# Performance work log

Measured on AMD Instinct MI355X. Metric: run time of the kernel, lower is better.

Reference implementation:

```python
import math
import jax, jax.numpy as jnp
import numpy as np

MARGIN_SCALER = 0.2
IGNORING_RATE = 0.1
NBITS = 64
TEMPERATURE = 0.1
B, L, E, D = 4096, 32, 512, 64


def setup_inputs() -> dict:
    key = jax.random.key(0)
    k1, k2, k3, k4, k5, k6 = jax.random.split(key, 6)
    return {
        "outputs_h1": jax.random.uniform(k1, (B, D), dtype=jnp.float32),
        "outputs_h2": jax.random.uniform(k2, (B, D), dtype=jnp.float32),
        "caps_embed": jax.random.normal(k3, (B, L, E), dtype=jnp.float32),
        "sim_mat": jax.random.normal(k4, (B, L, 1), dtype=jnp.float32),
        "s_v": jax.random.normal(k5, (B, D), dtype=jnp.float32),
        "s_v2": jax.random.normal(k6, (B, D), dtype=jnp.float32),
        "epochs": 5,
    }


def _cosine_sim(h, eps=1e-5):
    n = jnp.linalg.norm(h, axis=1, keepdims=True)
    a = h / jnp.maximum(n, eps)
    return a @ a.T  # [B, B]


def _self_contrastive_loss(img, tgt, caps_embed, epochs, sim_mat2d):
    batch_size = caps_embed.shape[0]
    w = jax.nn.softmax(sim_mat2d, axis=-1)              # [B, L]
    caps_mean = jnp.einsum('bl,ble->be', w, caps_embed)  # [B, E]
    cos = jnp.clip(_cosine_sim(caps_mean), 1e-6, 1.0 - 1e-6)  # [B, B]
    scores = img @ tgt.T                                 # [B, B]
    d1 = jnp.diag(scores)[:, None]
    cost_s = jnp.maximum((1.0 - cos) * MARGIN_SCALER + scores - d1, 1e-8)
    eye = jnp.eye(batch_size, dtype=cost_s.dtype)
    cost_s = cost_s * (1.0 - eye)  # masked_fill diagonal with 0
    clean_rate = epochs * IGNORING_RATE if epochs * IGNORING_RATE < 1 else 0.99
    k = math.ceil(batch_size * batch_size * (1 - clean_rate))
    thr = jnp.sort(cost_s.reshape(-1))[k - 1]  # k-th smallest (topk largest=False)
    cost_s = jnp.where(cost_s < thr, cost_s, jnp.zeros_like(cost_s))
    return cost_s.sum()


def _quantization_loss(img, nbits, lamda=1.0):
    loss = -lamda * jnp.sum((1.0 / nbits) * jnp.square(img - 0.5), axis=1)
    return loss.mean()


def _distillation_loss(stu, tcher, temperature=TEMPERATURE):
    p_t = jax.nn.log_softmax(tcher / temperature, axis=-1)
    p_s = jax.nn.log_softmax(stu / temperature, axis=-1)
    # KLDivLoss(reduction='sum', log_target=True): sum(exp(target)*(target-input))
    return jnp.sum(jnp.exp(p_t) * (p_t - p_s))


def reference(outputs_h1, outputs_h2, caps_embed, sim_mat, s_v, s_v2, epochs):
    sim2d = jax.lax.stop_gradient(sim_mat[..., 0])  # detach + squeeze(-1)
    loss1 = _self_contrastive_loss(outputs_h1, outputs_h2, caps_embed, epochs, sim2d)
    loss2 = _quantization_loss(outputs_h1, NBITS)
    loss3 = _distillation_loss(s_v2, s_v)
    # AutomaticWeightedLoss(3) with freshly-initialized params = ones(3):
    # sum_i 0.5/p_i^2 * loss_i + log(1 + p_i^2) with p_i = 1
    ln2 = jnp.log(jnp.asarray(2.0, dtype=jnp.float32))
    loss_sum = 0.5 * loss1 + ln2 + 0.5 * loss2 + ln2 + 0.5 * loss3 + ln2
    return loss_sum
```

## Files before the change

kernel.cpp:

```cpp
#include <hip/hip_runtime.h>
#include <hip/hip_bf16.h>

#define TPB 256
#define CTPB 512

using f32x4  = __attribute__((ext_vector_type(4))) float;
using bf16x8 = __attribute__((ext_vector_type(8))) short;

static constexpr int BB = 4096;

static constexpr size_t OFF_AHI  = 0;
static constexpr size_t OFF_D1   = 8388608;
static constexpr size_t OFF_H1   = OFF_D1 + 16384;
static constexpr size_t OFF_GS1  = OFF_H1 + 8192;
static constexpr size_t OFF_L2P  = OFF_GS1 + 16384;
static constexpr size_t OFF_L3P  = OFF_L2P + 8192;
static constexpr size_t OFF_HS   = OFF_L3P + 8192;
static constexpr size_t HS_ONE   = (size_t)BB * 64 * 2;
static constexpr size_t ZERO_OFF = OFF_H1;
static constexpr size_t ZERO_LEN = OFF_L2P - OFF_H1;

__device__ __forceinline__ void bsplit(float x, unsigned short& h, unsigned short& l)
{
    unsigned b = __float_as_uint(x);
    unsigned r = (b + 0x7FFFu + ((b >> 16) & 1u)) >> 16;
    h = (unsigned short)r;
    float hf = __uint_as_float(r << 16);
    float lof = x - hf;
    unsigned b2 = __float_as_uint(lof);
    unsigned r2 = (b2 + 0x7FFFu + ((b2 >> 16) & 1u)) >> 16;
    l = (unsigned short)r2;
}

__device__ __forceinline__ unsigned short b2h(float x)
{
    unsigned b = __float_as_uint(x);
    return (unsigned short)((b + 0x7FFFu + ((b >> 16) & 1u)) >> 16);
}

__device__ __forceinline__ void gload16(const void* g, void* l)
{
    __builtin_amdgcn_global_load_lds((const __attribute__((address_space(1))) void*)g,
                                     (__attribute__((address_space(3))) void*)l,
                                     16, 0, 0);
}

__global__ __launch_bounds__(TPB) void front_k(
    const float* __restrict__ caps, const float* __restrict__ sim,
    unsigned short* __restrict__ ahi,
    const float* __restrict__ h1f, const float* __restrict__ h2f,
    unsigned short* __restrict__ h1hi, unsigned short* __restrict__ h1lo,
    unsigned short* __restrict__ h2hi, unsigned short* __restrict__ h2lo,
    float* __restrict__ d1, const float* __restrict__ sv,
    const float* __restrict__ sv2, double* __restrict__ l2part,
    double* __restrict__ l3part, char* __restrict__ base)
{
    const int blk = (int)blockIdx.x;
    const int tid = threadIdx.x;
    __shared__ float sm[32];
    __shared__ float w[32];
    __shared__ float red[4];
    __shared__ float nrm;
    __shared__ double r2[4], r3[4];

    if (blk < 4096) {
        const int b = blk;
        if (tid < 32) sm[tid] = sim[b * 32 + tid];
        __syncthreads();
        if (tid < 32) {
            float m = -1e30f;
            for (int l = 0; l < 32; ++l) m = fmaxf(m, sm[l]);
            float ssum = 0.f;
            for (int l = 0; l < 32; ++l) ssum += expf(sm[l] - m);
            w[tid] = expf(sm[tid] - m) / ssum;
        }
        __syncthreads();
        const float2* cb2 = (const float2*)(caps + (size_t)b * 32 * 512);
        float cx = 0.f, cy = 0.f;
        for (int l = 0; l < 32; ++l) {
            float wl = w[l];
            float2 v = cb2[l * 256 + tid];
            cx = fmaf(wl, v.x, cx);
            cy = fmaf(wl, v.y, cy);
        }
        float ss = cx * cx + cy * cy;
        #pragma unroll
        for (int off = 32; off; off >>= 1) ss += __shfl_down(ss, off, 64);
        if ((tid & 63) == 0) red[tid >> 6] = ss;
        __syncthreads();
        if (tid == 0) nrm = sqrtf(red[0] + red[1] + red[2] + red[3]);
        __syncthreads();
        float an = fmaxf(nrm, 1e-5f);
        ahi[(size_t)b * 512 + 2 * tid]     = b2h(cx / an);
        ahi[(size_t)b * 512 + 2 * tid + 1] = b2h(cy / an);
    } else if (blk < 5120) {
        const int pb   = blk - 4096;
        const int row  = (pb << 2) + (tid >> 6);
        const int lane = tid & 63;
        const int i    = (row << 6) + lane;
        float x1 = h1f[i], x2 = h2f[i];
        unsigned short h, l;
        bsplit(x1, h, l); h1hi[i] = h; h1lo[i] = l;
        bsplit(x2, h, l); h2hi[i] = h; h2lo[i] = l;
        float p = x1 * x2;
        #pragma unroll
        for (int m = 32; m; m >>= 1) p += __shfl_xor(p, m, 64);
        if (lane == 0) d1[row] = p;
        float xq = x1 - 0.5f;
        double s2 = (double)(xq * xq);
        #pragma unroll
        for (int m = 32; m; m >>= 1) s2 += __shfl_xor(s2, m, 64);
        float xt = sv[i] / 0.1f;
        float xs = sv2[i] / 0.1f;
        float mt = xt, ms = xs;
        #pragma unroll
        for (int m = 32; m; m >>= 1) {
            mt = fmaxf(mt, __shfl_xor(mt, m, 64));
            ms = fmaxf(ms, __shfl_xor(ms, m, 64));
        }
        float et = expf(xt - mt), es = expf(xs - ms);
        float sst = et, sss = es;
        #pragma unroll
        for (int m = 32; m; m >>= 1) { sst += __shfl_xor(sst, m, 64); sss += __shfl_xor(sss, m, 64); }
        float pt = (xt - mt) - logf(sst);
        float ps = (xs - ms) - logf(sss);
        double d3 = (double)((et / sst) * (pt - ps));
        #pragma unroll
        for (int m = 32; m; m >>= 1) d3 += __shfl_xor(d3, m, 64);
        if (lane == 0) { r2[tid >> 6] = s2; r3[tid >> 6] = d3; }
        __syncthreads();
        if (tid == 0) {
            l2part[pb] = r2[0] + r2[1] + r2[2] + r2[3];
            l3part[pb] = r3[0] + r3[1] + r3[2] + r3[3];
        }
    } else {
        unsigned* z = (unsigned*)(base + ZERO_OFF);
        const int n = (int)(ZERO_LEN / 4);
        for (int i2 = (blk - 5120) * TPB + tid; i2 < n; i2 += 8 * TPB) z[i2] = 0u;
    }
}

__global__ __launch_bounds__(CTPB, 1) void cost_pass(
    const unsigned short* __restrict__ ahi,
    const unsigned short* __restrict__ h1hi, const unsigned short* __restrict__ h1lo,
    const unsigned short* __restrict__ h2hi, const unsigned short* __restrict__ h2lo,
    const float* __restrict__ d1,
    unsigned* __restrict__ hist, double* __restrict__ gsum)
{
    __shared__ char lds_raw[131072];
    __shared__ float sD1[128];
    const int tid  = threadIdx.x;
    const int lane = tid & 63;
    const int wid  = tid >> 6;
    const int wr   = wid >> 2;
    const int wc   = wid & 3;

    const int orig = (int)blockIdx.x;
    const int xcd  = orig & 7;
    const int idx  = orig >> 3;
    const int bi   = (((xcd >> 1) << 3) + (idx & 7)) << 7;
    const int bj   = (((xcd & 1) << 4) + (idx >> 3)) << 7;

    f32x4 accC[4][2], accS[4][2];
    #pragma unroll
    for (int m = 0; m < 4; ++m)
        #pragma unroll
        for (int n = 0; n < 2; ++n)
            #pragma unroll
            for (int q = 0; q < 4; ++q) { accC[m][n][q] = 0.f; accS[m][n][q] = 0.f; }

    auto STAGE = [&](int t) {
        char* d = lds_raw + ((size_t)(t & 3) << 15);
        if (t < 8) {
            const int k0b = t << 7;
            #pragma unroll
            for (int q = 0; q < 2; ++q) {
                int o    = (q << 13) + (tid << 4);
                int row  = o >> 7;
                int slot = (o >> 4) & 7;
                int sc   = (slot ^ (row & 7)) << 4;
                gload16((const char*)ahi + (size_t)(bi + row) * 1024 + k0b + sc, d + o);
                gload16((const char*)ahi + (size_t)(bj + row) * 1024 + k0b + sc, d + 16384 + o);
            }
        } else {
            const int k0b = (t - 8) << 6;
            int o    = tid << 4;
            int row  = o >> 6;
            int slot = (o >> 4) & 3;
            int sc   = (slot ^ ((row >> 1) & 3)) << 4;
            size_t ra = (size_t)(bi + row) * 128 + k0b + sc;
            size_t rb = (size_t)(bj + row) * 128 + k0b + sc;
            gload16((const char*)h1hi + ra, d + o);
            gload16((const char*)h1lo + ra, d + 8192 + o);
            gload16((const char*)h2hi + rb, d + 16384 + o);
            gload16((const char*)h2lo + rb, d + 24576 + o);
        }
    };

    STAGE(0);
    STAGE(1);
    #pragma unroll 1
    for (int t = 0; t < 10; ++t) {
        if (t < 8) STAGE(t + 2);
        __builtin_amdgcn_sched_barrier(0);
        if (t < 8)       asm volatile("s_waitcnt vmcnt(8)" ::: "memory");
        else if (t == 8) asm volatile("s_waitcnt vmcnt(4)" ::: "memory");
        else             asm volatile("s_waitcnt vmcnt(0)" ::: "memory");
        __builtin_amdgcn_s_barrier();
        const char* bufb = lds_raw + ((size_t)(t & 3) << 15);
        if (t < 8) {
            #pragma unroll
            for (int ks = 0; ks < 2; ++ks) {
                bf16x8 a_[4], b_[2];
                const int pbase = (ks << 2) + (lane >> 4);
                #pragma unroll
                for (int m = 0; m < 4; ++m) {
                    int row = wr * 64 + m * 16 + (lane & 15);
                    a_[m] = *(const bf16x8*)(bufb + row * 128 + ((pbase ^ (lane & 7)) << 4));
                }
                #pragma unroll
                for (int n = 0; n < 2; ++n) {
                    int row = wc * 32 + n * 16 + (lane & 15);
                    b_[n] = *(const bf16x8*)(bufb + 16384 + row * 128 + ((pbase ^ (lane & 7)) << 4));
                }
                __builtin_amdgcn_s_setprio(1);
                #pragma unroll
                for (int m = 0; m < 4; ++m)
                    #pragma unroll
                    for (int n = 0; n < 2; ++n)
                        accC[m][n] = __builtin_amdgcn_mfma_f32_16x16x32_bf16(a_[m], b_[n], accC[m][n], 0, 0, 0);
                __builtin_amdgcn_s_setprio(0);
            }
        } else {
            const int rdsw = (((lane >> 4) ^ ((lane >> 1) & 3)) << 4);
            bf16x8 ah[4], bh[2], bl[2];
            #pragma unroll
            for (int m = 0; m < 4; ++m)
                ah[m] = *(const bf16x8*)(bufb + (size_t)(wr * 64 + m * 16 + (lane & 15)) * 64 + rdsw);
            #pragma unroll
            for (int n = 0; n < 2; ++n) {
                bh[n] = *(const bf16x8*)(bufb + 16384 + (size_t)(wc * 32 + n * 16 + (lane & 15)) * 64 + rdsw);
                bl[n] = *(const bf16x8*)(bufb + 24576 + (size_t)(wc * 32 + n * 16 + (lane & 15)) * 64 + rdsw);
            }
            __builtin_amdgcn_s_setprio(1);
            #pragma unroll
            for (int m = 0; m < 4; ++m)
                #pragma unroll
                for (int n = 0; n < 2; ++n) {
                    accS[m][n] = __builtin_amdgcn_mfma_f32_16x16x32_bf16(ah[m], bh[n], accS[m][n], 0, 0, 0);
                    accS[m][n] = __builtin_amdgcn_mfma_f32_16x16x32_bf16(ah[m], bl[n], accS[m][n], 0, 0, 0);
                }
            __builtin_amdgcn_s_setprio(0);
            bf16x8 al[4];
            #pragma unroll
            for (int m = 0; m < 4; ++m)
                al[m] = *(const bf16x8*)(bufb + 8192 + (size_t)(wr * 64 + m * 16 + (lane & 15)) * 64 + rdsw);
            __builtin_amdgcn_s_setprio(1);
            #pragma unroll
            for (int m = 0; m < 4; ++m)
                #pragma unroll
                for (int n = 0; n < 2; ++n)
                    accS[m][n] = __builtin_amdgcn_mfma_f32_16x16x32_bf16(al[m], bh[n], accS[m][n], 0, 0, 0);
            __builtin_amdgcn_s_setprio(0);
        }
        __builtin_amdgcn_sched_barrier(0);
    }

    __syncthreads();
    unsigned* lh = (unsigned*)lds_raw;
    float*    ls = (float*)(lds_raw + 32768);
    if (tid < 128) sD1[tid] = d1[bi + tid];
    for (int q = tid; q < 8192; q += CTPB) lh[q] = 0u;
    for (int q = tid; q < 4096; q += CTPB) ls[q] = 0.f;
    __syncthreads();
    unsigned* lhW = lh + (wid >> 1) * 2048;
    float*    lsW = ls + (wid >> 2) * 2048;
    const unsigned CB = __float_as_uint(1e-8f);
    unsigned nclamp = 0;
    #pragma unroll
    for (int m = 0; m < 4; ++m) {
        #pragma unroll
        for (int r = 0; r < 4; ++r) {
            const int irow = wr * 64 + m * 16 + (lane >> 4) * 4 + r;
            const int i = bi + irow;
            const float di = sD1[irow];
            #pragma unroll
            for (int n = 0; n < 2; ++n) {
                const int j = bj + wc * 32 + n * 16 + (lane & 15);
                float cosv = fminf(fmaxf(accC[m][n][r], 1e-6f), 0.999999f);
                float v = (1.0f - cosv) * 0.2f + accS[m][n][r] - di;
                v = fmaxf(v, 1e-8f);
                if (i == j) v = 0.0f;
                unsigned bits = __float_as_uint(v);
                if (bits == CB) ++nclamp;
                else {
                    atomicAdd(&lhW[bits >> 21], 1u);
                    atomicAdd(&lsW[bits >> 21], v);
                }
            }
        }
    }
    if (nclamp) {
        atomicAdd(&lhW[CB >> 21], nclamp);
        atomicAdd(&lsW[CB >> 21], (float)((double)nclamp * 1e-8));
    }
    __syncthreads();
    for (int q = tid; q < 2048; q += CTPB) {
        unsigned c = lh[q] + lh[2048 + q] + lh[4096 + q] + lh[6144 + q];
        if (c) atomicAdd(&hist[q], c);
        float s = ls[q] + ls[2048 + q];
        if (s != 0.f) atomicAdd(&gsum[q], (double)s);
    }
}

__global__ __launch_bounds__(TPB) void scan_final(
    const unsigned* __restrict__ hist, const double* __restrict__ gsum,
    const int* __restrict__ epochs_ptr, const double* __restrict__ l2part,
    const double* __restrict__ l3part, float* __restrict__ out)
{
    const int tid = threadIdx.x;
    __shared__ unsigned wtot[4];
    __shared__ int sbin;
    __shared__ unsigned srem;
    __shared__ double dred[4], dred2[4], dred3[4];

    int e = epochs_ptr[0];
    if (e > 1000000 || e < 0) e = (int)__int_as_float(e);
    double cr = (double)e * 0.1;
    if (!(cr < 1.0)) cr = 0.99;
    double kd = ceil(16777216.0 * (1.0 - cr));
    if (kd < 1.0) kd = 1.0;
    if (kd > 16777216.0) kd = 16777216.0;
    unsigned k = (unsigned)kd;

    unsigned local[8];
    unsigned s = 0;
    #pragma unroll
    for (int r = 0; r < 8; ++r) { unsigned v = hist[tid * 8 + r]; local[r] = v; s += v; }
    unsigned inc = s;
    #pragma unroll
    for (int d = 1; d < 64; d <<= 1) {
        unsigned n = __shfl_up(inc, (unsigned)d, 64);
        if ((tid & 63) >= d) inc += n;
    }
    if ((tid & 63) == 63) wtot[tid >> 6] = inc;
    __syncthreads();
    unsigned woff = 0;
    for (int wv = 0; wv < (tid >> 6); ++wv) woff += wtot[wv];
    unsigned excl = woff + (inc - s);
    if (k > excl && k <= excl + s) {
        unsigned rem = k - excl;
        int bin = tid * 8;
        #pragma unroll
        for (int r = 0; r < 8; ++r) {
            if (rem <= local[r]) { bin = tid * 8 + r; break; }
            rem -= local[r];
        }
        sbin = bin; srem = rem;
    }
    __syncthreads();
    const int b1 = sbin;
    double s3 = 0.0, p2 = 0.0, p3 = 0.0;
    for (int q = tid; q < 2048; q += TPB) if (q < b1) s3 += gsum[q];
    for (int q = tid; q < 1024; q += TPB) { p2 += l2part[q]; p3 += l3part[q]; }
    #pragma unroll
    for (int off = 32; off; off >>= 1) {
        s3 += __shfl_down(s3, off, 64);
        p2 += __shfl_down(p2, off, 64);
        p3 += __shfl_down(p3, off, 64);
    }
    if ((tid & 63) == 0) { dred[tid >> 6] = s3; dred2[tid >> 6] = p2; dred3[tid >> 6] = p3; }
    __syncthreads();
    if (tid == 0) {
        double S1 = dred[0] + dred[1] + dred[2] + dred[3];
        double sum2 = dred2[0] + dred2[1] + dred2[2] + dred2[3];
        double sum3 = dred3[0] + dred3[1] + dred3[2] + dred3[3];
        unsigned cnt = hist[b1];
        unsigned rem = srem;
        double avg = (cnt > 0) ? (gsum[b1] / (double)cnt) : 0.0;
        double loss1 = S1 + (double)(rem - 1) * avg;
        double loss2 = -sum2 / (64.0 * 4096.0);
        double loss3 = sum3;
        double total = 0.5 * loss1 + 0.5 * loss2 + 0.5 * loss3
                     + 3.0 * 0.69314718055994530942;
        float v = (float)total;
        unsigned bits = __float_as_uint(v);
        unsigned lsb = (bits >> 16) & 1u;
        unsigned h = (bits + 0x7FFFu + lsb) >> 16;
        ((unsigned*)out)[0] = (bits & 0xFFFF0000u) | (h & 0xFFFFu);
    }
}

extern "C" void kernel_launch(void* const* d_in, const int* in_sizes, int n_in,
                              void* d_out, int out_size, void* d_ws, size_t ws_size,
                              hipStream_t stream) {
    const float* h1f  = (const float*)d_in[0];
    const float* h2f  = (const float*)d_in[1];
    const float* caps = (const float*)d_in[2];
    const float* sim  = (const float*)d_in[3];
    const float* sv   = (const float*)d_in[4];
    const float* sv2  = (const float*)d_in[5];
    const int*   ep   = (const int*)d_in[6];

    char* base = (char*)d_ws;
    unsigned short* AHI  = (unsigned short*)(base + OFF_AHI);
    float*    D1   = (float*)(base + OFF_D1);
    unsigned* H1   = (unsigned*)(base + OFF_H1);
    double*   GS1  = (double*)(base + OFF_GS1);
    double*   L2P  = (double*)(base + OFF_L2P);
    double*   L3P  = (double*)(base + OFF_L3P);
    unsigned short* H1HI = (unsigned short*)(base + OFF_HS);
    unsigned short* H1LO = (unsigned short*)(base + OFF_HS + HS_ONE);
    unsigned short* H2HI = (unsigned short*)(base + OFF_HS + 2 * HS_ONE);
    unsigned short* H2LO = (unsigned short*)(base + OFF_HS + 3 * HS_ONE);

    front_k<<<5128, TPB, 0, stream>>>(caps, sim, AHI, h1f, h2f,
                                      H1HI, H1LO, H2HI, H2LO, D1, sv, sv2,
                                      L2P, L3P, base);
    cost_pass<<<1024, CTPB, 0, stream>>>(AHI, H1HI, H1LO, H2HI, H2LO, D1, H1, GS1);
    scan_final<<<1, TPB, 0, stream>>>(H1, GS1, ep, L2P, L3P, (float*)d_out);
}
```

Before: 151.2 us.

## Exploit cosine matrix symmetry by computing only upper-triangular tile pairs

The cost pass now launches only the upper-triangular 128x128 tile pairs plus the diagonal tiles, 528 blocks instead of 1024. Each off-diagonal block computes the cosine Gram tile once and also computes both the h1·h2ᵀ and h2·h1ᵀ score tiles. The transposed cost values reuse the same cosine entries, which roughly halves the large E=512 cosine GEMM work. In exchange each off-diagonal block does two extra K-steps of split-bf16 MFMA, holds more accumulator registers, and does twice the histogram atomics. With 528 blocks on 256 CUs the load may also be uneven.

```diff
diff --git a/kernel.cpp b/kernel.cpp
--- a/kernel.cpp
+++ b/kernel.cpp
@@ -148,26 +148,36 @@
     unsigned* __restrict__ hist, double* __restrict__ gsum)
 {
     __shared__ char lds_raw[131072];
-    __shared__ float sD1[128];
+    __shared__ float sD1[256];
     const int tid  = threadIdx.x;
     const int lane = tid & 63;
     const int wid  = tid >> 6;
     const int wr   = wid >> 2;
     const int wc   = wid & 3;
 
-    const int orig = (int)blockIdx.x;
-    const int xcd  = orig & 7;
-    const int idx  = orig >> 3;
-    const int bi   = (((xcd >> 1) << 3) + (idx & 7)) << 7;
-    const int bj   = (((xcd & 1) << 4) + (idx >> 3)) << 7;
-
-    f32x4 accC[4][2], accS[4][2];
+    const int p = (int)blockIdx.x;
+    int ti, tj;
+    bool isDiag;
+    if (p < 496) {
+        isDiag = false;
+        int t0 = 0, rem = p;
+        while (rem >= 31 - t0) { rem -= 31 - t0; ++t0; }
+        ti = t0; tj = t0 + 1 + rem;
+    } else {
+        isDiag = true;
+        ti = tj = p - 496;
+    }
+    const int bi = ti << 7;
+    const int bj = tj << 7;
+    const int NR = isDiag ? 10 : 12;
+
+    f32x4 accC[4][2], accS1[4][2], accS2[4][2];
     #pragma unroll
     for (int m = 0; m < 4; ++m)
         #pragma unroll
         for (int n = 0; n < 2; ++n)
             #pragma unroll
-            for (int q = 0; q < 4; ++q) { accC[m][n][q] = 0.f; accS[m][n][q] = 0.f; }
+            for (int q = 0; q < 4; ++q) { accC[m][n][q] = 0.f; accS1[m][n][q] = 0.f; accS2[m][n][q] = 0.f; }
 
     auto STAGE = [&](int t) {
         char* d = lds_raw + ((size_t)(t & 3) << 15);
@@ -183,29 +193,34 @@
                 gload16((const char*)ahi + (size_t)(bj + row) * 1024 + k0b + sc, d + 16384 + o);
             }
         } else {
-            const int k0b = (t - 8) << 6;
+            const bool s1  = (t < 10);
+            const int  k0b = ((t - 8) & 1) << 6;
+            const char* Ahi = s1 ? (const char*)h1hi : (const char*)h2hi;
+            const char* Alo = s1 ? (const char*)h1lo : (const char*)h2lo;
+            const char* Bhi = s1 ? (const char*)h2hi : (const char*)h1hi;
+            const char* Blo = s1 ? (const char*)h2lo : (const char*)h1lo;
             int o    = tid << 4;
             int row  = o >> 6;
             int slot = (o >> 4) & 3;
             int sc   = (slot ^ ((row >> 1) & 3)) << 4;
             size_t ra = (size_t)(bi + row) * 128 + k0b + sc;
             size_t rb = (size_t)(bj + row) * 128 + k0b + sc;
-            gload16((const char*)h1hi + ra, d + o);
-            gload16((const char*)h1lo + ra, d + 8192 + o);
-            gload16((const char*)h2hi + rb, d + 16384 + o);
-            gload16((const char*)h2lo + rb, d + 24576 + o);
+            gload16(Ahi + ra, d + o);
+            gload16(Alo + ra, d + 8192 + o);
+            gload16(Bhi + rb, d + 16384 + o);
+            gload16(Blo + rb, d + 24576 + o);
         }
     };
 
     STAGE(0);
     STAGE(1);
     #pragma unroll 1
-    for (int t = 0; t < 10; ++t) {
-        if (t < 8) STAGE(t + 2);
+    for (int t = 0; t < NR; ++t) {
+        if (t < NR - 2) STAGE(t + 2);
         __builtin_amdgcn_sched_barrier(0);
-        if (t < 8)       asm volatile("s_waitcnt vmcnt(8)" ::: "memory");
-        else if (t == 8) asm volatile("s_waitcnt vmcnt(4)" ::: "memory");
-        else             asm volatile("s_waitcnt vmcnt(0)" ::: "memory");
+        if (t < NR - 2)       asm volatile("s_waitcnt vmcnt(8)" ::: "memory");
+        else if (t == NR - 2) asm volatile("s_waitcnt vmcnt(4)" ::: "memory");
+        else                  asm volatile("s_waitcnt vmcnt(0)" ::: "memory");
         __builtin_amdgcn_s_barrier();
         const char* bufb = lds_raw + ((size_t)(t & 3) << 15);
         if (t < 8) {
@@ -242,26 +257,33 @@
                 bh[n] = *(const bf16x8*)(bufb + 16384 + (size_t)(wc * 32 + n * 16 + (lane & 15)) * 64 + rdsw);
                 bl[n] = *(const bf16x8*)(bufb + 24576 + (size_t)(wc * 32 + n * 16 + (lane & 15)) * 64 + rdsw);
             }
-            __builtin_amdgcn_s_setprio(1);
-            #pragma unroll
-            for (int m = 0; m < 4; ++m)
-                #pragma unroll
-                for (int n = 0; n < 2; ++n) {
-                    accS[m][n] = __builtin_amdgcn_mfma_f32_16x16x32_bf16(ah[m], bh[n], accS[m][n], 0, 0, 0);
-                    accS[m][n] = __builtin_amdgcn_mfma_f32_16x16x32_bf16(ah[m], bl[n], accS[m][n], 0, 0, 0);
-                }
-            __builtin_amdgcn_s_setprio(0);
             bf16x8 al[4];
             #pragma unroll
             for (int m = 0; m < 4; ++m)
                 al[m] = *(const bf16x8*)(bufb + 8192 + (size_t)(wr * 64 + m * 16 + (lane & 15)) * 64 + rdsw);
-            __builtin_amdgcn_s_setprio(1);
-            #pragma unroll
-            for (int m = 0; m < 4; ++m)
+            if (t < 10) {
+                __builtin_amdgcn_s_setprio(1);
                 #pragma unroll
-                for (int n = 0; n < 2; ++n)
-                    accS[m][n] = __builtin_amdgcn_mfma_f32_16x16x32_bf16(al[m], bh[n], accS[m][n], 0, 0, 0);
-            __builtin_amdgcn_s_setprio(0);
+                for (int m = 0; m < 4; ++m)
+                    #pragma unroll
+                    for (int n = 0; n < 2; ++n) {
+                        accS1[m][n] = __builtin_amdgcn_mfma_f32_16x16x32_bf16(ah[m], bh[n], accS1[m][n], 0, 0, 0);
+                        accS1[m][n] = __builtin_amdgcn_mfma_f32_16x16x32_bf16(ah[m], bl[n], accS1[m][n], 0, 0, 0);
+                        accS1[m][n] = __builtin_amdgcn_mfma_f32_16x16x32_bf16(al[m], bh[n], accS1[m][n], 0, 0, 0);
+                    }
+                __builtin_amdgcn_s_setprio(0);
+            } else {
+                __builtin_amdgcn_s_setprio(1);
+                #pragma unroll
+                for (int m = 0; m < 4; ++m)
+                    #pragma unroll
+                    for (int n = 0; n < 2; ++n) {
+                        accS2[m][n] = __builtin_amdgcn_mfma_f32_16x16x32_bf16(ah[m], bh[n], accS2[m][n], 0, 0, 0);
+                        accS2[m][n] = __builtin_amdgcn_mfma_f32_16x16x32_bf16(ah[m], bl[n], accS2[m][n], 0, 0, 0);
+                        accS2[m][n] = __builtin_amdgcn_mfma_f32_16x16x32_bf16(al[m], bh[n], accS2[m][n], 0, 0, 0);
+                    }
+                __builtin_amdgcn_s_setprio(0);
+            }
         }
         __builtin_amdgcn_sched_barrier(0);
     }
@@ -270,6 +292,7 @@
     unsigned* lh = (unsigned*)lds_raw;
     float*    ls = (float*)(lds_raw + 32768);
     if (tid < 128) sD1[tid] = d1[bi + tid];
+    else if (tid < 256) sD1[tid] = d1[bj + tid - 128];
     for (int q = tid; q < 8192; q += CTPB) lh[q] = 0u;
     for (int q = tid; q < 4096; q += CTPB) ls[q] = 0.f;
     __syncthreads();
@@ -286,16 +309,27 @@
             const float di = sD1[irow];
             #pragma unroll
             for (int n = 0; n < 2; ++n) {
-                const int j = bj + wc * 32 + n * 16 + (lane & 15);
-                float cosv = fminf(fmaxf(accC[m][n][r], 1e-6f), 0.999999f);
-                float v = (1.0f - cosv) * 0.2f + accS[m][n][r] - di;
+                const int jcol = wc * 32 + n * 16 + (lane & 15);
+                const int j = bj + jcol;
+                float base01 = (1.0f - fminf(fmaxf(accC[m][n][r], 1e-6f), 0.999999f)) * 0.2f;
+                float v = base01 + accS1[m][n][r] - di;
                 v = fmaxf(v, 1e-8f);
-                if (i == j) v = 0.0f;
+                if (isDiag && i == j) v = 0.0f;
                 unsigned bits = __float_as_uint(v);
                 if (bits == CB) ++nclamp;
                 else {
                     atomicAdd(&lhW[bits >> 21], 1u);
                     atomicAdd(&lsW[bits >> 21], v);
+                }
+                if (!isDiag) {
+                    float v2 = base01 + accS2[m][n][r] - sD1[128 + jcol];
+                    v2 = fmaxf(v2, 1e-8f);
+                    unsigned bits2 = __float_as_uint(v2);
+                    if (bits2 == CB) ++nclamp;
+                    else {
+                        atomicAdd(&lhW[bits2 >> 21], 1u);
+                        atomicAdd(&lsW[bits2 >> 21], v2);
+                    }
                 }
             }
         }
@@ -417,6 +451,6 @@
     front_k<<<5128, TPB, 0, stream>>>(caps, sim, AHI, h1f, h2f,
                                       H1HI, H1LO, H2HI, H2LO, D1, sv, sv2,
                                       L2P, L3P, base);
-    cost_pass<<<1024, CTPB, 0, stream>>>(AHI, H1HI, H1LO, H2HI, H2LO, D1, H1, GS1);
+    cost_pass<<<528, CTPB, 0, stream>>>(AHI, H1HI, H1LO, H2HI, H2LO, D1, H1, GS1);
     scan_final<<<1, TPB, 0, stream>>>(H1, GS1, ep, L2P, L3P, (float*)d_out);
 }
```

Result: slower. 158.1 us (+4.6%).
